# Kernel optimization log

Measured on AMD Instinct MI355X. Metric: run time of the kernel, lower is better.

Reference implementation:

```python
import jax, jax.numpy as jnp
import numpy as np

P, N, GRID, C, S, STEPS, N_ADJ = 128, 512, 112, 64, 128, 3, 4
HW = GRID * GRID
IN_DIM = C + 2


def _ring_adjacency():
    # prepare_gcn_component builds a ring graph: each vertex connected to
    # n_adj nearest neighbors along the polygon, row-normalized.
    offs = np.concatenate([np.arange(1, N_ADJ // 2 + 1), -np.arange(1, N_ADJ // 2 + 1)])
    A = np.zeros((N, N), np.float32)
    idx = np.arange(N)
    for o in offs:
        A[idx, (idx + o) % N] = 1.0
    A /= A.sum(1, keepdims=True)
    return jnp.asarray(A)


def setup_inputs() -> dict:
    key = jax.random.key(0)
    ks = jax.random.split(key, 10)
    std = 0.01  # matches m.weight.data.normal_(0.0, 0.01)
    return {
        "feature": jax.random.normal(ks[0], (P, HW, C), jnp.float32),
        "init_polys": jax.random.uniform(ks[1], (P, N, 2), jnp.float32),
        "adj": _ring_adjacency(),
        "W1s": jax.random.normal(ks[2], (STEPS, IN_DIM, S), jnp.float32) * std,
        "W1n": jax.random.normal(ks[3], (STEPS, IN_DIM, S), jnp.float32) * std,
        "b1": jnp.zeros((STEPS, S), jnp.float32),
        "W2s": jax.random.normal(ks[4], (STEPS, S, S), jnp.float32) * std,
        "W2n": jax.random.normal(ks[5], (STEPS, S, S), jnp.float32) * std,
        "b2": jnp.zeros((STEPS, S), jnp.float32),
        "Wfc": jax.random.normal(ks[6], (STEPS, S, 2), jnp.float32) * std,
        "bfc": jnp.zeros((STEPS, 2), jnp.float32),
    }


def _gather(feat, ids):
    # feat: [P, HW, C], ids: [P, N] int -> [P, N, C]
    return jnp.take_along_axis(feat, ids[:, :, None], axis=1)


def _nearest_sample(feature, poly):
    # step-0 `sampling` path: gather at floor(coord*grid) flat indices
    X0 = jnp.clip(jnp.floor(poly[..., 0] * GRID), 0, GRID - 1)
    Y0 = jnp.clip(jnp.floor(poly[..., 1] * GRID), 0, GRID - 1)
    ids = (X0 + Y0 * GRID).astype(jnp.int32)
    return _gather(feature, ids)


def _interpolated_sum(feature, poly):
    Xs = poly[..., 0] * GRID
    Ys = poly[..., 1] * GRID
    X0 = jnp.floor(Xs); X1 = X0 + 1.0
    Y0 = jnp.floor(Ys); Y1 = Y0 + 1.0
    w00 = (X1 - Xs) * (Y1 - Ys)
    w01 = (X1 - Xs) * (Ys - Y0)
    w10 = (Xs - X0) * (Y1 - Ys)
    w11 = (Xs - X0) * (Ys - Y0)
    X0c = jnp.clip(X0, 0, GRID - 1).astype(jnp.int32)
    X1c = jnp.clip(X1, 0, GRID - 1).astype(jnp.int32)
    Y0c = jnp.clip(Y0, 0, GRID - 1).astype(jnp.int32)
    Y1c = jnp.clip(Y1, 0, GRID - 1).astype(jnp.int32)
    M00 = _gather(feature, X0c + Y0c * GRID)
    M01 = _gather(feature, X0c + Y1c * GRID)
    M10 = _gather(feature, X1c + Y0c * GRID)
    M11 = _gather(feature, X1c + Y1c * GRID)
    return (w00[..., None] * M00 + w01[..., None] * M01 +
            w10[..., None] * M10 + w11[..., None] * M11)


def _gconv(x, adj, Ws, Wn, b):
    # x: [P, N, D]; adj: [N, N] (shared ring graph)
    nbr = jnp.einsum('nm,pmd->pnd', adj, x)
    return x @ Ws + nbr @ Wn + b


def _gcn(x, adj, i, W1s, W1n, b1, W2s, W2n, b2, Wfc, bfc):
    h = jax.nn.relu(_gconv(x, adj, W1s[i], W1n[i], b1[i]))
    h = jax.nn.relu(_gconv(h, adj, W2s[i], W2n[i], b2[i]))
    return h @ Wfc[i] + bfc[i]  # [P, N, 2]


def reference(feature, init_polys, adj, W1s, W1n, b1, W2s, W2n, b2, Wfc, bfc):
    poly = init_polys
    for i in range(STEPS):
        cnn_feat = _nearest_sample(feature, poly) if i == 0 else _interpolated_sum(feature, poly)
        inp = jnp.concatenate([cnn_feat, poly], axis=2)  # [P, N, C+2]
        pred = _gcn(inp, adj, i, W1s, W1n, b1, W2s, W2n, b2, Wfc, bfc)
        poly = poly + pred
    return poly
```

## Files before the change

kernel.cpp:

```cpp
#include <hip/hip_runtime.h>

#define P_      128
#define NV      512
#define GRID_   112
#define HW_     (GRID_*GRID_)
#define C_      64
#define S_      128

typedef short bf16x8 __attribute__((ext_vector_type(8)));
typedef float f32x4  __attribute__((ext_vector_type(4)));

__device__ __forceinline__ unsigned short f2bf(float x) {
    union { float f; unsigned int u; } v; v.f = x;
    unsigned int r = (v.u + 0x7FFFu + ((v.u >> 16) & 1u)) >> 16;
    return (unsigned short)r;
}
__device__ __forceinline__ float2 up2(unsigned int u) {
    union { unsigned int u; float f; } a, b;
    a.u = u << 16; b.u = u & 0xFFFF0000u;
    return make_float2(a.f, b.f);
}
__device__ __forceinline__ unsigned int pk2(float lo, float hi) {
    return (unsigned int)f2bf(lo) | ((unsigned int)f2bf(hi) << 16);
}

__global__ __launch_bounds__(256) void wprep_kernel(
    const float* __restrict__ W1s, const float* __restrict__ W1n,
    const float* __restrict__ W2s, const float* __restrict__ W2n,
    unsigned short* __restrict__ W1p, unsigned short* __restrict__ W2p)
{
    int idx = blockIdx.x * 256 + threadIdx.x;
    const int N1 = 3 * 5 * 8 * 64 * 8;
    const int N2 = 3 * 8 * 8 * 64 * 8;
    if (idx < N1) {
        int j = idx & 7, lane = (idx >> 3) & 63, nt = (idx >> 9) & 7;
        int ks = (idx >> 12) % 5, step = idx / 20480;
        int n = nt * 16 + (lane & 15);
        int k = ks * 32 + (lane >> 4) * 8 + j;
        float v = 0.f;
        if (k < 66)       v = W1s[(step * 66 + k) * 128 + n];
        else if (k < 132) v = W1n[(step * 66 + (k - 66)) * 128 + n];
        W1p[idx] = f2bf(v);
    } else if (idx < N1 + N2) {
        int e = idx - N1;
        int j = e & 7, lane = (e >> 3) & 63, nt = (e >> 9) & 7;
        int ks = (e >> 12) & 7, step = e >> 15;
        int n = nt * 16 + (lane & 15);
        int k = ks * 32 + (lane >> 4) * 8 + j;
        float v = (k < 128) ? W2s[(step * 128 + k) * 128 + n]
                            : W2n[(step * 128 + (k - 128)) * 128 + n];
        W2p[e] = f2bf(v);
    }
}

#define X_BYTES 38976
#define Y_BYTES 33792
__global__ __launch_bounds__(256) void step_kernel(
    const float* __restrict__ feature,
    const float* __restrict__ poly_in,
    const unsigned short* __restrict__ W1p,
    const float* __restrict__ b1,
    const unsigned short* __restrict__ W2p,
    const float* __restrict__ b2,
    const float* __restrict__ Wfc, const float* __restrict__ bfc,
    float* __restrict__ poly_out,
    int nearest)
{
    __shared__ __align__(16) char smem[X_BYTES + Y_BYTES];
    unsigned int*   raw_u = (unsigned int*)smem;
    unsigned int*   A1_u  = (unsigned int*)(smem + 12096);
    unsigned short* h1s   = (unsigned short*)smem;
    unsigned int*   A2_u  = (unsigned int*)(smem + X_BYTES);
    float*          h2    = (float*)(smem + X_BYTES);

    int p  = blockIdx.x >> 3;
    int n0 = (blockIdx.x & 7) * 64;
    int wv = threadIdx.x >> 6, lane = threadIdx.x & 63;
    int m = lane & 15, q = lane >> 4;

    const float* fb = feature + (size_t)p * HW_ * C_;
    const float* pp = poly_in + (size_t)p * NV * 2;
    for (int r = wv; r < 84; r += 4) {
        int n = (n0 + r - 10) & (NV - 1);
        float px = pp[2 * n], py = pp[2 * n + 1];
        float val;
        if (nearest) {
            float X0 = fminf(fmaxf(floorf(px * (float)GRID_), 0.f), (float)(GRID_ - 1));
            float Y0 = fminf(fmaxf(floorf(py * (float)GRID_), 0.f), (float)(GRID_ - 1));
            int id = (int)X0 + (int)Y0 * GRID_;
            val = fb[(size_t)id * C_ + lane];
        } else {
            float Xs = px * (float)GRID_, Ys = py * (float)GRID_;
            float X0 = floorf(Xs), Y0 = floorf(Ys);
            float X1 = X0 + 1.f, Y1 = Y0 + 1.f;
            float ax = X1 - Xs, bx = Xs - X0;
            float ay = Y1 - Ys, by = Ys - Y0;
            int X0c = (int)fminf(fmaxf(X0, 0.f), (float)(GRID_ - 1));
            int X1c = (int)fminf(fmaxf(X1, 0.f), (float)(GRID_ - 1));
            int Y0c = (int)fminf(fmaxf(Y0, 0.f), (float)(GRID_ - 1));
            int Y1c = (int)fminf(fmaxf(Y1, 0.f), (float)(GRID_ - 1));
            float m00 = fb[(size_t)(X0c + Y0c * GRID_) * C_ + lane];
            float m01 = fb[(size_t)(X0c + Y1c * GRID_) * C_ + lane];
            float m10 = fb[(size_t)(X1c + Y0c * GRID_) * C_ + lane];
            float m11 = fb[(size_t)(X1c + Y1c * GRID_) * C_ + lane];
            val = (ax * ay) * m00 + (ax * by) * m01 + (bx * ay) * m10 + (bx * by) * m11;
        }
        unsigned short* row = (unsigned short*)raw_u + r * 72;
        row[lane] = f2bf(val);
        if (lane < 8)
            row[64 + lane] = (lane == 0) ? f2bf(px) : (lane == 1) ? f2bf(py) : 0;
    }
    __syncthreads();

    for (int idx = threadIdx.x; idx < 80 * 84; idx += 256) {
        int a = idx / 84, u = idx - a * 84;
        unsigned int val;
        if (u < 33) {
            val = raw_u[(a + 2) * 36 + u];
        } else if (u < 66) {
            int uu = u - 33;
            float2 fa = up2(raw_u[a * 36 + uu]),       fb2 = up2(raw_u[(a + 1) * 36 + uu]);
            float2 fc = up2(raw_u[(a + 3) * 36 + uu]), fd  = up2(raw_u[(a + 4) * 36 + uu]);
            val = pk2(0.25f * (fa.x + fb2.x + fc.x + fd.x),
                      0.25f * (fa.y + fb2.y + fc.y + fd.y));
        } else val = 0u;
        A1_u[idx] = val;
    }
    __syncthreads();

    f32x4 acc1[10];
    #pragma unroll
    for (int i = 0; i < 10; i++) acc1[i] = (f32x4){0.f, 0.f, 0.f, 0.f};
    const bf16x8* B1 = (const bf16x8*)W1p;
    #pragma unroll
    for (int i = 0; i < 10; i++) {
        int t = wv * 10 + i;
        int mt = t >> 3, nt = t & 7;
        const unsigned short* arow = (const unsigned short*)A1_u + (mt * 16 + m) * 168 + q * 8;
        #pragma unroll
        for (int ks = 0; ks < 5; ks++) {
            bf16x8 a = *(const bf16x8*)(arow + ks * 32);
            bf16x8 b = B1[(ks * 8 + nt) * 64 + lane];
            acc1[i] = __builtin_amdgcn_mfma_f32_16x16x32_bf16(a, b, acc1[i], 0, 0, 0);
        }
    }
    __syncthreads();

    #pragma unroll
    for (int i = 0; i < 10; i++) {
        int t = wv * 10 + i;
        int mt = t >> 3, nt = t & 7;
        int col = nt * 16 + m;
        float bias = b1[col];
        #pragma unroll
        for (int rg = 0; rg < 4; rg++) {
            int row = mt * 16 + q * 4 + rg;
            h1s[row * 132 + col] = f2bf(fmaxf(acc1[i][rg] + bias, 0.f));
        }
    }
    __syncthreads();

    const unsigned int* h1u = (const unsigned int*)h1s;
    for (int idx = threadIdx.x; idx < 64 * 128; idx += 256) {
        int a = idx >> 7, u = idx & 127;
        unsigned int val;
        if (u < 64) {
            val = h1u[(a + 8) * 66 + u];
        } else {
            int uu = u - 64;
            float2 fa = up2(h1u[(a + 6) * 66 + uu]), fb2 = up2(h1u[(a + 7) * 66 + uu]);
            float2 fc = up2(h1u[(a + 9) * 66 + uu]), fd  = up2(h1u[(a + 10) * 66 + uu]);
            val = pk2(0.25f * (fa.x + fb2.x + fc.x + fd.x),
                      0.25f * (fa.y + fb2.y + fc.y + fd.y));
        }
        A2_u[(a * 132) + u] = val;
    }
    __syncthreads();

    f32x4 acc2[8];
    #pragma unroll
    for (int nt = 0; nt < 8; nt++) acc2[nt] = (f32x4){0.f, 0.f, 0.f, 0.f};
    const bf16x8* B2 = (const bf16x8*)W2p;
    const unsigned short* arow2 = (const unsigned short*)A2_u + (wv * 16 + m) * 264 + q * 8;
    #pragma unroll
    for (int ks = 0; ks < 8; ks++) {
        bf16x8 a = *(const bf16x8*)(arow2 + ks * 32);
        #pragma unroll
        for (int nt = 0; nt < 8; nt++) {
            bf16x8 b = B2[(ks * 8 + nt) * 64 + lane];
            acc2[nt] = __builtin_amdgcn_mfma_f32_16x16x32_bf16(a, b, acc2[nt], 0, 0, 0);
        }
    }
    __syncthreads();

    #pragma unroll
    for (int nt = 0; nt < 8; nt++) {
        int col = nt * 16 + m;
        float bias = b2[col];
        #pragma unroll
        for (int rg = 0; rg < 4; rg++) {
            int row = wv * 16 + q * 4 + rg;
            h2[row * 129 + col] = fmaxf(acc2[nt][rg] + bias, 0.f);
        }
    }
    __syncthreads();

    if (threadIdx.x < 128) {
        int v = threadIdx.x >> 1, j = threadIdx.x & 1;
        float pr = bfc[j];
        const float* hv = h2 + v * 129;
        #pragma unroll 4
        for (int c = 0; c < 128; c++) pr += hv[c] * Wfc[c * 2 + j];
        size_t o = ((size_t)p * NV + n0 + v) * 2 + j;
        poly_out[o] = poly_in[o] + pr;
    }
}

extern "C" void kernel_launch(void* const* d_in, const int* in_sizes, int n_in,
                              void* d_out, int out_size, void* d_ws, size_t ws_size,
                              hipStream_t stream)
{
    const float* feature    = (const float*)d_in[0];
    const float* init_polys = (const float*)d_in[1];
    const float* W1s = (const float*)d_in[3];
    const float* W1n = (const float*)d_in[4];
    const float* b1  = (const float*)d_in[5];
    const float* W2s = (const float*)d_in[6];
    const float* W2n = (const float*)d_in[7];
    const float* b2  = (const float*)d_in[8];
    const float* Wfc = (const float*)d_in[9];
    const float* bfc = (const float*)d_in[10];
    float* out = (float*)d_out;

    char* wsb = (char*)d_ws;
    float* polyA = (float*)wsb;                  wsb += (size_t)P_ * NV * 2 * 4;
    float* polyB = (float*)wsb;                  wsb += (size_t)P_ * NV * 2 * 4;
    unsigned short* W1p = (unsigned short*)wsb;  wsb += (size_t)61440 * 2;
    unsigned short* W2p = (unsigned short*)wsb;

    wprep_kernel<<<624, 256, 0, stream>>>(W1s, W1n, W2s, W2n, W1p, W2p);

    const float* pin = init_polys;
    for (int i = 0; i < 3; i++) {
        float* pout = (i == 2) ? out : ((i == 0) ? polyA : polyB);
        step_kernel<<<P_ * 8, 256, 0, stream>>>(
            feature, pin,
            W1p + (size_t)i * 20480, b1 + i * 128,
            W2p + (size_t)i * 32768, b2 + i * 128,
            Wfc + i * 256, bfc + i * 2,
            pout, i == 0);
        pin = pout;
    }
}
```

Before: 699.9 us.

## Split sampling into separate kernel to remove redundant halo gathers

Sampling of feature values is moved into its own kernel that writes bf16 vertex inputs to a workspace, so each vertex is gathered once instead of being resampled in overlapping halos by neighbouring blocks. The GCN kernel then loads a smaller 4-row halo from the workspace, cutting shared-memory use and A1/A2 sizes. The final FC projection is spread over all threads with a shuffle reduction. This adds an extra launch per step and a global round trip for the intermediate.

```diff
diff --git a/kernel.cpp b/kernel.cpp
--- a/kernel.cpp
+++ b/kernel.cpp
@@ -53,77 +53,84 @@
     }
 }
 
-#define X_BYTES 38976
-#define Y_BYTES 33792
-__global__ __launch_bounds__(256) void step_kernel(
-    const float* __restrict__ feature,
-    const float* __restrict__ poly_in,
+__global__ __launch_bounds__(256) void sample_kernel(
+    const float* __restrict__ feature, const float* __restrict__ poly,
+    unsigned short* __restrict__ inp, int nearest)
+{
+    int w = threadIdx.x >> 6, lane = threadIdx.x & 63;
+    int g = blockIdx.x * 4 + w;
+    int p = g >> 9;
+    float px = poly[2 * g], py = poly[2 * g + 1];
+    const float* fb = feature + (size_t)p * HW_ * C_;
+    float val;
+    if (nearest) {
+        float X0 = fminf(fmaxf(floorf(px * (float)GRID_), 0.f), (float)(GRID_ - 1));
+        float Y0 = fminf(fmaxf(floorf(py * (float)GRID_), 0.f), (float)(GRID_ - 1));
+        int id = (int)X0 + (int)Y0 * GRID_;
+        val = fb[(size_t)id * C_ + lane];
+    } else {
+        float Xs = px * (float)GRID_, Ys = py * (float)GRID_;
+        float X0 = floorf(Xs), Y0 = floorf(Ys);
+        float X1 = X0 + 1.f, Y1 = Y0 + 1.f;
+        float ax = X1 - Xs, bx = Xs - X0;
+        float ay = Y1 - Ys, by = Ys - Y0;
+        int X0c = (int)fminf(fmaxf(X0, 0.f), (float)(GRID_ - 1));
+        int X1c = (int)fminf(fmaxf(X1, 0.f), (float)(GRID_ - 1));
+        int Y0c = (int)fminf(fmaxf(Y0, 0.f), (float)(GRID_ - 1));
+        int Y1c = (int)fminf(fmaxf(Y1, 0.f), (float)(GRID_ - 1));
+        float m00 = fb[(size_t)(X0c + Y0c * GRID_) * C_ + lane];
+        float m01 = fb[(size_t)(X0c + Y1c * GRID_) * C_ + lane];
+        float m10 = fb[(size_t)(X1c + Y0c * GRID_) * C_ + lane];
+        float m11 = fb[(size_t)(X1c + Y1c * GRID_) * C_ + lane];
+        val = (ax * ay) * m00 + (ax * by) * m01 + (bx * ay) * m10 + (bx * by) * m11;
+    }
+    unsigned short* row = inp + (size_t)g * 72;
+    row[lane] = f2bf(val);
+    if (lane < 8)
+        row[64 + lane] = (lane == 0) ? f2bf(px) : (lane == 1) ? f2bf(py) : 0;
+}
+
+__global__ __launch_bounds__(256) void gcn_kernel(
+    const unsigned short* __restrict__ inp,
     const unsigned short* __restrict__ W1p,
     const float* __restrict__ b1,
     const unsigned short* __restrict__ W2p,
     const float* __restrict__ b2,
     const float* __restrict__ Wfc, const float* __restrict__ bfc,
-    float* __restrict__ poly_out,
-    int nearest)
-{
-    __shared__ __align__(16) char smem[X_BYTES + Y_BYTES];
+    const float* __restrict__ poly_in, float* __restrict__ poly_out)
+{
+    __shared__ __align__(16) char smem[54400];
     unsigned int*   raw_u = (unsigned int*)smem;
-    unsigned int*   A1_u  = (unsigned int*)(smem + 12096);
+    unsigned int*   A1_u  = (unsigned int*)(smem + 10368);
     unsigned short* h1s   = (unsigned short*)smem;
-    unsigned int*   A2_u  = (unsigned int*)(smem + X_BYTES);
-    float*          h2    = (float*)(smem + X_BYTES);
-
-    int p  = blockIdx.x >> 3;
-    int n0 = (blockIdx.x & 7) * 64;
+    unsigned int*   A2_u  = (unsigned int*)(smem + 21120);
+    float*          h2    = (float*)(smem + 21120);
+
+    int p = blockIdx.x >> 3, n0 = (blockIdx.x & 7) * 64;
     int wv = threadIdx.x >> 6, lane = threadIdx.x & 63;
     int m = lane & 15, q = lane >> 4;
 
-    const float* fb = feature + (size_t)p * HW_ * C_;
-    const float* pp = poly_in + (size_t)p * NV * 2;
-    for (int r = wv; r < 84; r += 4) {
-        int n = (n0 + r - 10) & (NV - 1);
-        float px = pp[2 * n], py = pp[2 * n + 1];
-        float val;
-        if (nearest) {
-            float X0 = fminf(fmaxf(floorf(px * (float)GRID_), 0.f), (float)(GRID_ - 1));
-            float Y0 = fminf(fmaxf(floorf(py * (float)GRID_), 0.f), (float)(GRID_ - 1));
-            int id = (int)X0 + (int)Y0 * GRID_;
-            val = fb[(size_t)id * C_ + lane];
-        } else {
-            float Xs = px * (float)GRID_, Ys = py * (float)GRID_;
-            float X0 = floorf(Xs), Y0 = floorf(Ys);
-            float X1 = X0 + 1.f, Y1 = Y0 + 1.f;
-            float ax = X1 - Xs, bx = Xs - X0;
-            float ay = Y1 - Ys, by = Ys - Y0;
-            int X0c = (int)fminf(fmaxf(X0, 0.f), (float)(GRID_ - 1));
-            int X1c = (int)fminf(fmaxf(X1, 0.f), (float)(GRID_ - 1));
-            int Y0c = (int)fminf(fmaxf(Y0, 0.f), (float)(GRID_ - 1));
-            int Y1c = (int)fminf(fmaxf(Y1, 0.f), (float)(GRID_ - 1));
-            float m00 = fb[(size_t)(X0c + Y0c * GRID_) * C_ + lane];
-            float m01 = fb[(size_t)(X0c + Y1c * GRID_) * C_ + lane];
-            float m10 = fb[(size_t)(X1c + Y0c * GRID_) * C_ + lane];
-            float m11 = fb[(size_t)(X1c + Y1c * GRID_) * C_ + lane];
-            val = (ax * ay) * m00 + (ax * by) * m01 + (bx * ay) * m10 + (bx * by) * m11;
-        }
-        unsigned short* row = (unsigned short*)raw_u + r * 72;
-        row[lane] = f2bf(val);
-        if (lane < 8)
-            row[64 + lane] = (lane == 0) ? f2bf(px) : (lane == 1) ? f2bf(py) : 0;
+    const unsigned int* inpu = (const unsigned int*)inp + (size_t)p * NV * 36;
+    for (int idx = threadIdx.x; idx < 72 * 36; idx += 256) {
+        int r = idx / 36, u = idx - r * 36;
+        raw_u[idx] = inpu[(size_t)((n0 + r - 4) & 511) * 36 + u];
     }
     __syncthreads();
 
     for (int idx = threadIdx.x; idx < 80 * 84; idx += 256) {
         int a = idx / 84, u = idx - a * 84;
-        unsigned int val;
-        if (u < 33) {
-            val = raw_u[(a + 2) * 36 + u];
-        } else if (u < 66) {
-            int uu = u - 33;
-            float2 fa = up2(raw_u[a * 36 + uu]),       fb2 = up2(raw_u[(a + 1) * 36 + uu]);
-            float2 fc = up2(raw_u[(a + 3) * 36 + uu]), fd  = up2(raw_u[(a + 4) * 36 + uu]);
-            val = pk2(0.25f * (fa.x + fb2.x + fc.x + fd.x),
-                      0.25f * (fa.y + fb2.y + fc.y + fd.y));
-        } else val = 0u;
+        unsigned int val = 0u;
+        if (a < 68) {
+            if (u < 33) {
+                val = raw_u[(a + 2) * 36 + u];
+            } else if (u < 66) {
+                int uu = u - 33;
+                float2 fa = up2(raw_u[a * 36 + uu]),       fb2 = up2(raw_u[(a + 1) * 36 + uu]);
+                float2 fc = up2(raw_u[(a + 3) * 36 + uu]), fd  = up2(raw_u[(a + 4) * 36 + uu]);
+                val = pk2(0.25f * (fa.x + fb2.x + fc.x + fd.x),
+                          0.25f * (fa.y + fb2.y + fc.y + fd.y));
+            }
+        }
         A1_u[idx] = val;
     }
     __syncthreads();
@@ -165,15 +172,15 @@
         int a = idx >> 7, u = idx & 127;
         unsigned int val;
         if (u < 64) {
-            val = h1u[(a + 8) * 66 + u];
+            val = h1u[(a + 2) * 66 + u];
         } else {
             int uu = u - 64;
-            float2 fa = up2(h1u[(a + 6) * 66 + uu]), fb2 = up2(h1u[(a + 7) * 66 + uu]);
-            float2 fc = up2(h1u[(a + 9) * 66 + uu]), fd  = up2(h1u[(a + 10) * 66 + uu]);
+            float2 fa = up2(h1u[a * 66 + uu]),       fb2 = up2(h1u[(a + 1) * 66 + uu]);
+            float2 fc = up2(h1u[(a + 3) * 66 + uu]), fd  = up2(h1u[(a + 4) * 66 + uu]);
             val = pk2(0.25f * (fa.x + fb2.x + fc.x + fd.x),
                       0.25f * (fa.y + fb2.y + fc.y + fd.y));
         }
-        A2_u[(a * 132) + u] = val;
+        A2_u[a * 130 + u] = val;
     }
     __syncthreads();
 
@@ -181,7 +188,7 @@
     #pragma unroll
     for (int nt = 0; nt < 8; nt++) acc2[nt] = (f32x4){0.f, 0.f, 0.f, 0.f};
     const bf16x8* B2 = (const bf16x8*)W2p;
-    const unsigned short* arow2 = (const unsigned short*)A2_u + (wv * 16 + m) * 264 + q * 8;
+    const unsigned short* arow2 = (const unsigned short*)A2_u + (wv * 16 + m) * 260 + q * 8;
     #pragma unroll
     for (int ks = 0; ks < 8; ks++) {
         bf16x8 a = *(const bf16x8*)(arow2 + ks * 32);
@@ -205,14 +212,20 @@
     }
     __syncthreads();
 
-    if (threadIdx.x < 128) {
-        int v = threadIdx.x >> 1, j = threadIdx.x & 1;
-        float pr = bfc[j];
-        const float* hv = h2 + v * 129;
-        #pragma unroll 4
-        for (int c = 0; c < 128; c++) pr += hv[c] * Wfc[c * 2 + j];
-        size_t o = ((size_t)p * NV + n0 + v) * 2 + j;
-        poly_out[o] = poly_in[o] + pr;
+    {
+        int t = threadIdx.x;
+        int oi = t >> 1, half = t & 1;
+        int v = oi >> 1, j = oi & 1;
+        float pr = half ? 0.f : bfc[j];
+        const float* hv = h2 + v * 129 + half * 64;
+        #pragma unroll 8
+        for (int cc = 0; cc < 64; cc++)
+            pr += hv[cc] * Wfc[(half * 64 + cc) * 2 + j];
+        pr += __shfl_xor(pr, 1);
+        if (half == 0) {
+            size_t o = ((size_t)p * NV + n0 + v) * 2 + j;
+            poly_out[o] = poly_in[o] + pr;
+        }
     }
 }
 
@@ -236,19 +249,20 @@
     float* polyA = (float*)wsb;                  wsb += (size_t)P_ * NV * 2 * 4;
     float* polyB = (float*)wsb;                  wsb += (size_t)P_ * NV * 2 * 4;
     unsigned short* W1p = (unsigned short*)wsb;  wsb += (size_t)61440 * 2;
-    unsigned short* W2p = (unsigned short*)wsb;
+    unsigned short* W2p = (unsigned short*)wsb;  wsb += (size_t)98304 * 2;
+    unsigned short* inp = (unsigned short*)wsb;
 
     wprep_kernel<<<624, 256, 0, stream>>>(W1s, W1n, W2s, W2n, W1p, W2p);
 
     const float* pin = init_polys;
     for (int i = 0; i < 3; i++) {
         float* pout = (i == 2) ? out : ((i == 0) ? polyA : polyB);
-        step_kernel<<<P_ * 8, 256, 0, stream>>>(
-            feature, pin,
-            W1p + (size_t)i * 20480, b1 + i * 128,
+        sample_kernel<<<P_ * NV / 4, 256, 0, stream>>>(feature, pin, inp, i == 0);
+        gcn_kernel<<<P_ * 8, 256, 0, stream>>>(
+            inp, W1p + (size_t)i * 20480, b1 + i * 128,
             W2p + (size_t)i * 32768, b2 + i * 128,
             Wfc + i * 256, bfc + i * 2,
-            pout, i == 0);
+            pin, pout);
         pin = pout;
     }
 }
```

Result: faster. 644.1 us (-8.0%).
